# Kernel tuning notes

Hardware: AMD Instinct MI355X
Metric: run time of the kernel (lower is better)

## Reference

```python
import jax, jax.numpy as jnp
import numpy as np

# Irreps config: node = 64x0e + 32x1o, edge sh = 1x0e + 1x1o
N, E = 50000, 800000
MUL0, MUL1 = 64, 32
D_IN = MUL0 + 3 * MUL1          # 160
FC_H = 64
W_NUMEL = MUL0 + MUL0 + MUL1 + MUL1  # 192, per-instruction uvu weights
SQRT3 = 1.7320508075688772
ACT_C = 1.6791   # e3nn normalize2mom constant for silu


def setup_inputs() -> dict:
    key = jax.random.key(0)
    ks = jax.random.split(key, 11)
    return {
        "x": jax.random.normal(ks[0], (N, D_IN), jnp.float32),
        "edge_scalars": jax.random.uniform(ks[1], (E, FC_H), dtype=jnp.float32),
        "edge_attr_sh": jax.random.normal(ks[2], (E, 4), jnp.float32),
        "edge_index": jax.random.randint(ks[3], (2, E), 0, N),
        "w_fc1": jax.random.normal(ks[4], (FC_H, FC_H), jnp.float32),
        "w_fc2": jax.random.normal(ks[5], (FC_H, W_NUMEL), jnp.float32),
        "w_sc_s": jax.random.normal(ks[6], (MUL0, MUL0), jnp.float32),
        "w_sc_v": jax.random.normal(ks[7], (MUL1, MUL1), jnp.float32),
        "w_lin_s": jax.random.normal(ks[8], (96, MUL0), jnp.float32),
        "w_lin_v": jax.random.normal(ks[9], (96, MUL1), jnp.float32),
        "w_alpha": jax.random.normal(ks[10], (96, 1), jnp.float32) * 0.1,
    }


def reference(x, edge_scalars, edge_attr_sh, edge_index, w_fc1, w_fc2,
              w_sc_s, w_sc_v, w_lin_s, w_lin_v, w_alpha):
    src, dst = edge_index[0], edge_index[1]

    # --- fc: FullyConnectedNet([64, 64, 192], silu), e3nn fan-in norm ---
    h = jax.nn.silu(edge_scalars @ w_fc1 / np.sqrt(FC_H)) * ACT_C
    weight = h @ w_fc2 / np.sqrt(FC_H)                       # [E, 192]
    w0 = weight[:, :MUL0]                 # 0e x 0e -> 0e (mul 64)
    w1 = weight[:, MUL0:2 * MUL0]         # 0e x 1o -> 1o (mul 64)
    w2 = weight[:, 2 * MUL0:2 * MUL0 + MUL1]   # 1o x 0e -> 1o (mul 32)
    w3 = weight[:, 2 * MUL0 + MUL1:]           # 1o x 1o -> 0e (mul 32)

    # --- self connection: o3.Linear(in -> out), per-irrep mixing ---
    x_s = x[:, :MUL0]                                   # [N, 64]
    x_v = x[:, MUL0:].reshape(N, MUL1, 3)               # [N, 32, 3]
    sc_s = x_s @ w_sc_s / np.sqrt(MUL0)
    sc_v = jnp.einsum('nui,uw->nwi', x_v, w_sc_v) / np.sqrt(MUL1)
    sc_out = jnp.concatenate([sc_s, sc_v.reshape(N, 3 * MUL1)], axis=1)

    # --- gather + edge-weighted uvu tensor product ---
    gx_s = x_s[src]                                     # [E, 64]
    gx_v = x_v[src]                                     # [E, 32, 3]
    sh_s = edge_attr_sh[:, 0:1]                         # [E, 1]
    sh_v = edge_attr_sh[:, 1:4]                         # [E, 3]

    # path weights fold with w3j so factors cancel for 1o outputs
    mid_s0 = w0 * gx_s * sh_s                                        # [E,64] 0e
    mid_s1 = w3 * jnp.einsum('eui,ei->eu', gx_v, sh_v) / SQRT3       # [E,32] 0e
    mid_v0 = w1[:, :, None] * gx_s[:, :, None] * sh_v[:, None, :]    # [E,64,3] 1o
    mid_v1 = w2[:, :, None] * gx_v * sh_s[:, :, None]                # [E,32,3] 1o
    edge_feat = jnp.concatenate(
        [mid_s0, mid_s1, mid_v0.reshape(E, 3 * MUL0), mid_v1.reshape(E, 3 * MUL1)],
        axis=1)                                                      # [E, 384]

    # --- scatter-mean to destination nodes ---
    seg = jax.ops.segment_sum(edge_feat, dst, num_segments=N)
    cnt = jax.ops.segment_sum(jnp.ones((E,), edge_feat.dtype), dst, num_segments=N)
    mean = seg / jnp.maximum(cnt, 1.0)[:, None]                      # [N, 384]

    m_s = mean[:, :96]                                   # 96x0e
    m_v = mean[:, 96:].reshape(N, 96, 3)                 # 96x1o

    # --- alpha gate (o3.Linear mid -> 0e) and output linear ---
    alpha = m_s @ w_alpha / np.sqrt(96)                  # [N, 1]
    lin_s = m_s @ w_lin_s / np.sqrt(96)                  # [N, 64]
    lin_v = jnp.einsum('nui,uw->nwi', m_v, w_lin_v) / np.sqrt(96)
    lin_out = jnp.concatenate([lin_s, lin_v.reshape(N, 3 * MUL1)], axis=1)

    # sc.output_mask is all-ones here (every output irrep reachable)
    return sc_out + alpha * lin_out
```

## Files before the change

### kernel.cpp

```cpp
#include <hip/hip_runtime.h>
#include <hip/hip_bf16.h>

#define N_NODES 50000
#define N_EDGES 800000
#define MUL0 64
#define MUL1 32
#define D_IN 160
#define FC_H 64
#define W_NUMEL 192
#define FEAT 384
#define ACT_C 1.6791f
#define INV_SQRT3 0.57735026918962576f
#define RSQRT32 0.17677669529663687f
#define RSQRT96 0.10206207261596575f

#define TILE 32

typedef __attribute__((ext_vector_type(8))) short s16x8;
typedef __attribute__((ext_vector_type(4))) float f32x4;
typedef _Float16 h8 __attribute__((ext_vector_type(8)));
typedef __fp16 fp16x2 __attribute__((ext_vector_type(2)));

static __device__ __forceinline__ unsigned short f2bf(float f) {
    __hip_bfloat16 b = __float2bfloat16(f);
    return __builtin_bit_cast(unsigned short, b);
}

static __device__ __forceinline__ int swz(int row, int byte_in_row) {
    int unit = ((row & 1) << 2) | (byte_in_row >> 4);
    int su = unit ^ ((row >> 1) & 7);
    return (row >> 1) * 128 + su * 16 + (byte_in_row & 15);
}
static __device__ __forceinline__ h8 rdh8(const unsigned char* base, int row, int eb) {
    return *(const h8*)(base + swz(row, eb));
}


__global__ __launch_bounds__(256) void hist_kernel(const int* __restrict__ eidx,
                                                   int* __restrict__ cnt) {
    int e = blockIdx.x * 256 + threadIdx.x;
    if (e < N_EDGES) atomicAdd(&cnt[eidx[N_EDGES + e]], 1);
}

#define SCAN_NB 64
#define SCAN_CH ((N_NODES + SCAN_NB - 1) / SCAN_NB)

__global__ __launch_bounds__(256) void scanA_kernel(const int* __restrict__ cnt,
                                                    int* __restrict__ bsum) {
    __shared__ int sred[4];
    int b = blockIdx.x, t = threadIdx.x;
    int lim = min((b + 1) * SCAN_CH, N_NODES);
    int s = 0;
    for (int i = b * SCAN_CH + t; i < lim; i += 256) s += cnt[i];
    for (int d = 1; d < 64; d <<= 1) s += __shfl_xor(s, d);
    if ((t & 63) == 0) sred[t >> 6] = s;
    __syncthreads();
    if (t == 0) bsum[b] = sred[0] + sred[1] + sred[2] + sred[3];
}

__global__ __launch_bounds__(64) void scanB_kernel(const int* __restrict__ bsum,
                                                   int* __restrict__ boff) {
    int t = threadIdx.x;
    int v = bsum[t];
    int p = v;
    for (int d = 1; d < 64; d <<= 1) { int u = __shfl_up(p, d); if (t >= d) p += u; }
    boff[t] = p - v;
}

__global__ __launch_bounds__(256) void scanC_kernel(const int* __restrict__ cnt,
                                                    const int* __restrict__ boff,
                                                    int* __restrict__ fill) {
    __shared__ int s_w[4];
    int b = blockIdx.x, t = threadIdx.x;
    const int CH2 = (SCAN_CH + 255) / 256;
    int base = b * SCAN_CH + t * CH2;
    int lim = min((b + 1) * SCAN_CH, N_NODES);
    int s = 0;
#pragma unroll
    for (int k = 0; k < CH2; ++k) { int i = base + k; if (i < lim) s += cnt[i]; }
    int v = s;
    for (int d = 1; d < 64; d <<= 1) { int u = __shfl_up(v, d); if ((t & 63) >= d) v += u; }
    if ((t & 63) == 63) s_w[t >> 6] = v;
    __syncthreads();
    if (t == 0) { int run = 0; for (int w = 0; w < 4; ++w) { int tv = s_w[w]; s_w[w] = run; run += tv; } }
    __syncthreads();
    int run = boff[b] + s_w[t >> 6] + (v - s);
#pragma unroll
    for (int k = 0; k < CH2; ++k) {
        int i = base + k;
        if (i < lim) { fill[i] = run; run += cnt[i]; }
    }
}

__global__ __launch_bounds__(256) void scatter_ids_kernel(const int* __restrict__ eidx,
                                                          int* __restrict__ fill,
                                                          int* __restrict__ sorted_eid) {
    int e = blockIdx.x * 256 + threadIdx.x;
    if (e < N_EDGES) {
        int p = atomicAdd(&fill[eidx[N_EDGES + e]], 1);
        sorted_eid[p] = e;
    }
}

__global__ __launch_bounds__(256) void prep_w_kernel(
    const float* __restrict__ w_fc1,
    const float* __restrict__ w_fc2,
    const float* __restrict__ w_sc_s,
    const float* __restrict__ w_sc_v,
    const float* __restrict__ w_lin_s,
    const float* __restrict__ w_lin_v,
    unsigned short* __restrict__ w1t,
    unsigned short* __restrict__ w2t,
    unsigned short* __restrict__ wscs_t,
    unsigned short* __restrict__ wscv_t,
    unsigned short* __restrict__ wlins_t,
    unsigned short* __restrict__ wlinv_t)
{
    int i = blockIdx.x * 256 + threadIdx.x;
    if (i < 64 * 64)  w1t[i]    = f2bf(w_fc1[(i & 63) * FC_H + (i >> 6)]);
    if (i < 192 * 64) w2t[i]    = f2bf(w_fc2[(i & 63) * W_NUMEL + (i >> 6)]);
    if (i < 64 * 64)  wscs_t[i] = f2bf(w_sc_s[(i & 63) * 64 + (i >> 6)]);
    if (i < 32 * 32)  wscv_t[i] = f2bf(w_sc_v[(i & 31) * 32 + (i >> 5)]);
    if (i < 64 * 96)  wlins_t[i] = f2bf(w_lin_s[(i % 96) * 64 + (i / 96)]);
    if (i < 32 * 96)  wlinv_t[i] = f2bf(w_lin_v[(i % 96) * 32 + (i / 96)]);
}

#define X_OFF    0
#define W_OFF    10240
#define SH_OFF   22528
#define SID_OFF  22784
#define SEGN_OFF 22848
#define NSEG_OFF 22976
#define SMEM_SZ  22980

static __device__ __forceinline__ h8 seg_mask(const unsigned* vv, unsigned tgt) {
    h8 a;
#pragma unroll
    for (int w2 = 0; w2 < 4; ++w2) {
        a[w2 * 2]     = ((vv[w2] & 0xffffu) == tgt) ? (_Float16)1.f : (_Float16)0.f;
        a[w2 * 2 + 1] = ((vv[w2] >> 16)     == tgt) ? (_Float16)1.f : (_Float16)0.f;
    }
    return a;
}

__global__ __launch_bounds__(256) void edge_kernel(
    const float* __restrict__ x,
    const float* __restrict__ es,
    const float* __restrict__ sh,
    const int*   __restrict__ eidx,
    const int*   __restrict__ sorted_eid,
    const unsigned short* __restrict__ w1t,
    const unsigned short* __restrict__ w2t,
    float* __restrict__ accg)
{
    __shared__ __align__(16) unsigned char smem[SMEM_SZ];
    int* s_segnode = (int*)(smem + SEGN_OFF);
    unsigned short* s_sid = (unsigned short*)(smem + SID_OFF);

    const int t = threadIdx.x;
    const int l = t & 63;
    const int wv = t >> 6;
    const int lr = l & 15;
    const int lk = l >> 4;
    const int rg   = wv & 1;
    const int half = wv >> 1;
    const int tile0 = blockIdx.x * TILE;

    s16x8 w1b[2][2];
#pragma unroll
    for (int j = 0; j < 2; ++j)
#pragma unroll
        for (int kk = 0; kk < 2; ++kk)
            w1b[j][kk] = *(const s16x8*)(w1t + ((half * 2 + j) * 16 + lr) * 64 + kk * 32 + lk * 8);

    int eid_own = sorted_eid[tile0 + rg * 16 + lr];
    float4 esf[4];
    {
        const float4* ep = (const float4*)(es + (size_t)eid_own * FC_H);
        esf[0] = ep[lk * 2];     esf[1] = ep[lk * 2 + 1];
        esf[2] = ep[8 + lk * 2]; esf[3] = ep[8 + lk * 2 + 1];
    }
    const int xe = l & 31;
    const int xc0 = (wv * 2 + (l >> 5)) * 5;
    const int src_e = eidx[sorted_eid[tile0 + xe]];
    float4 xg[5];
    {
        const float4* xp = (const float4*)(x + (size_t)src_e * D_IN);
#pragma unroll
        for (int k = 0; k < 5; ++k) xg[k] = xp[xc0 + k];
    }
    float shv = 0.f;
    if (t < 128) shv = sh[(size_t)sorted_eid[tile0 + (t >> 2)] * 4 + (t & 3)];
    if (wv == 0) {
        int dl = (l < 32) ? eidx[N_EDGES + sorted_eid[tile0 + l]] : -1;
        int nd = __shfl_down(dl, 1);
        bool flag = (l == 31) || (l < 31 && dl != nd);
        unsigned long long m = __ballot(flag) & 0xffffffffull;
        int sid = __popcll(m & ((1ull << l) - 1ull));
        if (l < 32) {
            s_sid[l] = (unsigned short)sid;
            if (flag) s_segnode[sid] = dl;
            if (l == 31) *(int*)(smem + NSEG_OFF) = sid + 1;
        }
    }

    unsigned short* s_h = (unsigned short*)(smem + X_OFF);
    s16x8 afrag[2];
    {
        s16x8 a;
        a[0] = f2bf(esf[0].x); a[1] = f2bf(esf[0].y); a[2] = f2bf(esf[0].z); a[3] = f2bf(esf[0].w);
        a[4] = f2bf(esf[1].x); a[5] = f2bf(esf[1].y); a[6] = f2bf(esf[1].z); a[7] = f2bf(esf[1].w);
        afrag[0] = a;
        a[0] = f2bf(esf[2].x); a[1] = f2bf(esf[2].y); a[2] = f2bf(esf[2].z); a[3] = f2bf(esf[2].w);
        a[4] = f2bf(esf[3].x); a[5] = f2bf(esf[3].y); a[6] = f2bf(esf[3].z); a[7] = f2bf(esf[3].w);
        afrag[1] = a;
    }
#pragma unroll
    for (int j = 0; j < 2; ++j) {
        int nt = half * 2 + j;
        f32x4 hacc = {0.f, 0.f, 0.f, 0.f};
#pragma unroll
        for (int kk = 0; kk < 2; ++kk)
            hacc = __builtin_amdgcn_mfma_f32_16x16x32_bf16(afrag[kk], w1b[j][kk], hacc, 0, 0, 0);
#pragma unroll
        for (int q = 0; q < 4; ++q) {
            float aa = hacc[q] * 0.125f;
            float hv = aa * (1.f / (1.f + __expf(-aa))) * ACT_C;
            s_h[(rg * 16 + lk * 4 + q) * 72 + nt * 16 + lr] = f2bf(hv);
        }
    }
    __syncthreads();

    s16x8 hfrag[2];
#pragma unroll
    for (int kk = 0; kk < 2; ++kk)
        hfrag[kk] = *(const s16x8*)(s_h + (rg * 16 + lr) * 72 + kk * 32 + lk * 8);
    __syncthreads();

#pragma unroll
    for (int j = 0; j < 6; ++j) {
        int nt = half * 6 + j;
        f32x4 acc = {0.f, 0.f, 0.f, 0.f};
#pragma unroll
        for (int kk = 0; kk < 2; ++kk) {
            s16x8 b = *(const s16x8*)(w2t + (nt * 16 + lr) * 64 + kk * 32 + lk * 8);
            acc = __builtin_amdgcn_mfma_f32_16x16x32_bf16(hfrag[kk], b, acc, 0, 0, 0);
        }
        int f = nt * 16 + lr;
        fp16x2 p0 = __builtin_amdgcn_cvt_pkrtz(acc[0] * 0.125f, acc[1] * 0.125f);
        fp16x2 p1 = __builtin_amdgcn_cvt_pkrtz(acc[2] * 0.125f, acc[3] * 0.125f);
        uint2 wval = { __builtin_bit_cast(unsigned, p0), __builtin_bit_cast(unsigned, p1) };
        *(uint2*)(smem + W_OFF + swz(f, rg * 32 + lk * 8)) = wval;
    }
#pragma unroll
    for (int k = 0; k < 5; ++k) {
        float4 v = xg[k];
#pragma unroll
        for (int jj = 0; jj < 4; ++jj) {
            int r = (xc0 + k) * 4 + jj;
            float fv = (jj == 0) ? v.x : (jj == 1) ? v.y : (jj == 2) ? v.z : v.w;
            *(_Float16*)(smem + X_OFF + swz(r, xe * 2)) = (_Float16)fv;
        }
    }
    if (t < 128) {
        int e = t >> 2, c = t & 3;
        *(_Float16*)(smem + SH_OFF + swz(c, e * 2)) = (_Float16)shv;
    }
    __syncthreads();

    const int nseg = *(const int*)(smem + NSEG_OFF);
    const int eb = lk * 16;

    h8 shreg[4];
#pragma unroll
    for (int r = 0; r < 4; ++r) shreg[r] = rdh8(smem + SH_OFF, r, eb);
    uint4 sv = *(const uint4*)(smem + SID_OFF + eb);
    unsigned vv[4] = { sv.x, sv.y, sv.z, sv.w };

    h8 Bv[4];
    int fcol[4];
    bool cls3j[4] = {false, false, false, false};
    if (wv == 0) {
#pragma unroll
        for (int jj = 0; jj < 4; ++jj) {
            int col = jj * 16 + lr;
            Bv[jj] = rdh8(smem + W_OFF, col, eb) * rdh8(smem + X_OFF, col, eb);
            fcol[jj] = col;
        }
    } else if (wv == 1) {
#pragma unroll
        for (int jj = 0; jj < 4; ++jj) {
            int col = jj * 16 + lr;
            Bv[jj] = rdh8(smem + W_OFF, 128 + col / 3, eb) * rdh8(smem + X_OFF, 64 + col, eb);
            fcol[jj] = 288 + col;
        }
    } else if (wv == 2) {
#pragma unroll
        for (int jj = 0; jj < 2; ++jj) {
            int col = 64 + jj * 16 + lr;
            Bv[jj] = rdh8(smem + W_OFF, 128 + col / 3, eb) * rdh8(smem + X_OFF, 64 + col, eb);
            fcol[jj] = 288 + col;
        }
#pragma unroll
        for (int jj = 2; jj < 4; ++jj) {
            int col = (jj - 2) * 16 + lr;
            h8 d = rdh8(smem + X_OFF, 64 + 3 * col, eb)     * shreg[1]
                 + rdh8(smem + X_OFF, 64 + 3 * col + 1, eb) * shreg[2]
                 + rdh8(smem + X_OFF, 64 + 3 * col + 2, eb) * shreg[3];
            Bv[jj] = rdh8(smem + W_OFF, 160 + col, eb) * d;
            fcol[jj] = 64 + col;
            cls3j[jj] = true;
        }
    } else {
#pragma unroll
        for (int jj = 0; jj < 4; ++jj) {
            int col = jj * 16 + lr;
            Bv[jj] = rdh8(smem + W_OFF, 64 + col, eb) * rdh8(smem + X_OFF, col, eb);
            fcol[jj] = 96 + 3 * col;
        }
    }

    if (wv != 3) {
        const int npass = (nseg + 15) >> 4;
        for (int p = 0; p < npass; ++p) {
            h8 bm = seg_mask(vv, (unsigned)(p * 16 + lr));
            h8 Ash = bm * shreg[0];
            const int m0 = p * 16 + lk * 4;
            float* nptr[4]; bool valid[4], atq[4];
#pragma unroll
            for (int q = 0; q < 4; ++q) {
                int sg = m0 + q;
                valid[q] = sg < nseg;
                int node = valid[q] ? s_segnode[sg] : 0;
                nptr[q] = accg + (size_t)node * FEAT;
                atq[q] = (sg == 0) || (sg == nseg - 1);
            }
#pragma unroll
            for (int jj = 0; jj < 4; ++jj) {
                f32x4 acc = {0.f, 0.f, 0.f, 0.f};
                acc = __builtin_amdgcn_mfma_f32_16x16x32_f16(cls3j[jj] ? bm : Ash, Bv[jj], acc, 0, 0, 0);
                const float sc = cls3j[jj] ? INV_SQRT3 : 1.f;
#pragma unroll
                for (int q = 0; q < 4; ++q) {
                    if (valid[q]) {
                        float v = acc[q] * sc;
                        float* a = nptr[q] + fcol[jj];
                        if (atq[q]) atomicAdd(a, v); else *a = v;
                    }
                }
            }
        }
    } else {
        const int npass = (3 * nseg + 15) >> 4;
        for (int p = 0; p < npass; ++p) {
            int m = p * 16 + lr;
            int sgA = m / 3, i3A = m - 3 * sgA;
            h8 A = seg_mask(vv, (unsigned)sgA) *
                   ((i3A == 0) ? shreg[1] : (i3A == 1) ? shreg[2] : shreg[3]);
            int m0 = p * 16 + lk * 4;
            int sgq = m0 / 3, rq = m0 - 3 * sgq;
            float* nptr[4]; int i3q[4]; bool valid[4], atq[4];
#pragma unroll
            for (int q = 0; q < 4; ++q) {
                valid[q] = sgq < nseg;
                int node = valid[q] ? s_segnode[sgq] : 0;
                nptr[q] = accg + (size_t)node * FEAT;
                i3q[q] = rq;
                atq[q] = (sgq == 0) || (sgq == nseg - 1);
                if (++rq == 3) { rq = 0; ++sgq; }
            }
#pragma unroll
            for (int jj = 0; jj < 4; ++jj) {
                f32x4 acc = {0.f, 0.f, 0.f, 0.f};
                acc = __builtin_amdgcn_mfma_f32_16x16x32_f16(A, Bv[jj], acc, 0, 0, 0);
#pragma unroll
                for (int q = 0; q < 4; ++q) {
                    if (valid[q]) {
                        float* a = nptr[q] + fcol[jj] + i3q[q];
                        if (atq[q]) atomicAdd(a, acc[q]); else *a = acc[q];
                    }
                }
            }
        }
    }
}


static __device__ __forceinline__ s16x8 frag_c8(const float* p, float s) {
    float4 u = *(const float4*)p, v = *(const float4*)(p + 4);
    s16x8 a;
    a[0] = f2bf(u.x * s); a[1] = f2bf(u.y * s); a[2] = f2bf(u.z * s); a[3] = f2bf(u.w * s);
    a[4] = f2bf(v.x * s); a[5] = f2bf(v.y * s); a[6] = f2bf(v.z * s); a[7] = f2bf(v.w * s);
    return a;
}

__global__ __launch_bounds__(256) void node_kernel(
    const float* __restrict__ x,
    const float* __restrict__ accg,
    const int*   __restrict__ cnt,
    const unsigned short* __restrict__ wscs_t,
    const unsigned short* __restrict__ wscv_t,
    const unsigned short* __restrict__ wlins_t,
    const unsigned short* __restrict__ wlinv_t,
    const float* __restrict__ w_alpha,
    float* __restrict__ out)
{
    const int t = threadIdx.x;
    const int wv = t >> 6, l = t & 63;
    const int lr = l & 15, lk = l >> 4;
    const int n_base = blockIdx.x * 64 + wv * 16;
    const int nrow = n_base + lr;
    const int nclamp = min(nrow, N_NODES - 1);

    const float* mrow = accg + (size_t)nclamp * FEAT;
    const float* xrow = x + (size_t)nclamp * D_IN;
    const float rinv = 1.f / (float)max(cnt[nclamp], 1);

    s16x8 ax[2], ams[3], axv[3], amv[3][3];
#pragma unroll
    for (int kk = 0; kk < 2; ++kk) ax[kk] = frag_c8(xrow + kk * 32 + lk * 8, 1.f);
#pragma unroll
    for (int kk = 0; kk < 3; ++kk) ams[kk] = frag_c8(mrow + kk * 32 + lk * 8, rinv);
    {
        float xb[24];
        const float4* p = (const float4*)(xrow + 64 + 24 * lk);
#pragma unroll
        for (int q = 0; q < 6; ++q) ((float4*)xb)[q] = p[q];
#pragma unroll
        for (int i = 0; i < 3; ++i) {
            s16x8 a;
#pragma unroll
            for (int j = 0; j < 8; ++j) a[j] = f2bf(xb[3 * j + i]);
            axv[i] = a;
        }
    }
#pragma unroll
    for (int kk = 0; kk < 3; ++kk) {
        float mb[24];
        const float4* p = (const float4*)(mrow + 96 + 96 * kk + 24 * lk);
#pragma unroll
        for (int q = 0; q < 6; ++q) ((float4*)mb)[q] = p[q];
#pragma unroll
        for (int i = 0; i < 3; ++i) {
            s16x8 a;
#pragma unroll
            for (int j = 0; j < 8; ++j) a[j] = f2bf(mb[3 * j + i] * rinv);
            amv[i][kk] = a;
        }
    }

    float ap = 0.f;
    {
        float ab[24];
        const float4* p = (const float4*)(mrow + 24 * lk);
#pragma unroll
        for (int q = 0; q < 6; ++q) ((float4*)ab)[q] = p[q];
#pragma unroll
        for (int j = 0; j < 24; ++j) ap += ab[j] * rinv * w_alpha[lk * 24 + j];
    }
    ap += __shfl_xor(ap, 16);
    ap += __shfl_xor(ap, 32);
    const float alphav = ap * RSQRT96;

    f32x4 accA[4], accL[4];
#pragma unroll
    for (int nt = 0; nt < 4; ++nt) { accA[nt] = (f32x4){0,0,0,0}; accL[nt] = (f32x4){0,0,0,0}; }
#pragma unroll
    for (int nt = 0; nt < 4; ++nt) {
#pragma unroll
        for (int kk = 0; kk < 2; ++kk) {
            s16x8 b = *(const s16x8*)(wscs_t + (nt * 16 + lr) * 64 + kk * 32 + lk * 8);
            accA[nt] = __builtin_amdgcn_mfma_f32_16x16x32_bf16(ax[kk], b, accA[nt], 0, 0, 0);
        }
#pragma unroll
        for (int kk = 0; kk < 3; ++kk) {
            s16x8 b = *(const s16x8*)(wlins_t + (nt * 16 + lr) * 96 + kk * 32 + lk * 8);
            accL[nt] = __builtin_amdgcn_mfma_f32_16x16x32_bf16(ams[kk], b, accL[nt], 0, 0, 0);
        }
    }
    f32x4 accVs[3][2], accVl[3][2];
#pragma unroll
    for (int i = 0; i < 3; ++i)
#pragma unroll
        for (int nt = 0; nt < 2; ++nt) { accVs[i][nt] = (f32x4){0,0,0,0}; accVl[i][nt] = (f32x4){0,0,0,0}; }
#pragma unroll
    for (int i = 0; i < 3; ++i) {
#pragma unroll
        for (int nt = 0; nt < 2; ++nt) {
            s16x8 b = *(const s16x8*)(wscv_t + (nt * 16 + lr) * 32 + lk * 8);
            accVs[i][nt] = __builtin_amdgcn_mfma_f32_16x16x32_bf16(axv[i], b, accVs[i][nt], 0, 0, 0);
#pragma unroll
            for (int kk = 0; kk < 3; ++kk) {
                s16x8 b2 = *(const s16x8*)(wlinv_t + (nt * 16 + lr) * 96 + kk * 32 + lk * 8);
                accVl[i][nt] = __builtin_amdgcn_mfma_f32_16x16x32_bf16(amv[i][kk], b2, accVl[i][nt], 0, 0, 0);
            }
        }
    }

#pragma unroll
    for (int q = 0; q < 4; ++q) {
        int row = lk * 4 + q;
        float ar = __shfl(alphav, row);
        int n = n_base + row;
        bool ok = (n < N_NODES);
        float* orow = out + (size_t)n * 160;
#pragma unroll
        for (int nt = 0; nt < 4; ++nt) {
            float vout = accA[nt][q] * 0.125f + ar * accL[nt][q] * RSQRT96;
            if (ok) orow[nt * 16 + lr] = vout;
        }
#pragma unroll
        for (int i = 0; i < 3; ++i)
#pragma unroll
            for (int nt = 0; nt < 2; ++nt) {
                float vout = accVs[i][nt][q] * RSQRT32 + ar * accVl[i][nt][q] * RSQRT96;
                if (ok) orow[64 + 3 * (nt * 16 + lr) + i] = vout;
            }
    }
}


extern "C" void kernel_launch(void* const* d_in, const int* in_sizes, int n_in,
                              void* d_out, int out_size, void* d_ws, size_t ws_size,
                              hipStream_t stream) {
    const float* x        = (const float*)d_in[0];
    const float* es       = (const float*)d_in[1];
    const float* sh       = (const float*)d_in[2];
    const int*   eidx     = (const int*)d_in[3];
    const float* w_fc1    = (const float*)d_in[4];
    const float* w_fc2    = (const float*)d_in[5];
    const float* w_sc_s   = (const float*)d_in[6];
    const float* w_sc_v   = (const float*)d_in[7];
    const float* w_lin_s  = (const float*)d_in[8];
    const float* w_lin_v  = (const float*)d_in[9];
    const float* w_alpha  = (const float*)d_in[10];
    float* out = (float*)d_out;

    float* accg       = (float*)d_ws;
    int*   cnt        = (int*)(accg + (size_t)N_NODES * FEAT);
    int*   fill       = cnt + N_NODES;
    int*   sorted_eid = fill + N_NODES;
    unsigned short* w1t     = (unsigned short*)(sorted_eid + N_EDGES);
    unsigned short* w2t     = w1t + 64 * 64;
    unsigned short* wscs_t  = w2t + 192 * 64;
    unsigned short* wscv_t  = wscs_t + 64 * 64;
    unsigned short* wlins_t = wscv_t + 32 * 32;
    unsigned short* wlinv_t = wlins_t + 64 * 96;
    int* bsum = (int*)(wlinv_t + 32 * 96);
    int* boff = bsum + SCAN_NB;

    (void)hipMemsetAsync(d_ws, 0, ((size_t)N_NODES * FEAT + N_NODES) * 4, stream);
    hipLaunchKernelGGL(hist_kernel, dim3((N_EDGES + 255) / 256), dim3(256), 0, stream,
                       eidx, cnt);
    hipLaunchKernelGGL(scanA_kernel, dim3(SCAN_NB), dim3(256), 0, stream, cnt, bsum);
    hipLaunchKernelGGL(scanB_kernel, dim3(1), dim3(64), 0, stream, bsum, boff);
    hipLaunchKernelGGL(scanC_kernel, dim3(SCAN_NB), dim3(256), 0, stream, cnt, boff, fill);
    hipLaunchKernelGGL(scatter_ids_kernel, dim3((N_EDGES + 255) / 256), dim3(256), 0, stream,
                       eidx, fill, sorted_eid);
    hipLaunchKernelGGL(prep_w_kernel, dim3(48), dim3(256), 0, stream,
                       w_fc1, w_fc2, w_sc_s, w_sc_v, w_lin_s, w_lin_v,
                       w1t, w2t, wscs_t, wscv_t, wlins_t, wlinv_t);
    hipLaunchKernelGGL(edge_kernel, dim3(N_EDGES / TILE), dim3(256), 0, stream,
                       x, es, sh, eidx, sorted_eid, w1t, w2t, accg);
    hipLaunchKernelGGL(node_kernel, dim3((N_NODES + 63) / 64), dim3(256), 0, stream,
                       x, accg, cnt, wscs_t, wscv_t, wlins_t, wlinv_t, w_alpha, out);
}
```

Baseline: 475.1 us.

## Double edge tile to 64 edges per block with two-step K segment reduction

Raises the per-block edge tile from 32 to 64. Each wave now computes the fc MLP for its own 16-edge row group across all output columns, and the segment-reduction MFMA runs two K-steps over the 64 edges. The shared-memory swizzle and layout are reworked for 64-edge rows. The aim is fewer segments that straddle tile boundaries, so fewer atomics, and fewer blocks overall. In exchange the block roughly doubles its LDS footprint and register use, which may lower occupancy.

New measurement: 453.0 us. 1.05x faster.

```diff
diff --git a/kernel.cpp b/kernel.cpp
--- a/kernel.cpp
+++ b/kernel.cpp
@@ -14,7 +14,7 @@
 #define RSQRT32 0.17677669529663687f
 #define RSQRT96 0.10206207261596575f
 
-#define TILE 32
+#define TILE 64
 
 typedef __attribute__((ext_vector_type(8))) short s16x8;
 typedef __attribute__((ext_vector_type(4))) float f32x4;
@@ -27,9 +27,7 @@
 }
 
 static __device__ __forceinline__ int swz(int row, int byte_in_row) {
-    int unit = ((row & 1) << 2) | (byte_in_row >> 4);
-    int su = unit ^ ((row >> 1) & 7);
-    return (row >> 1) * 128 + su * 16 + (byte_in_row & 15);
+    return row * 128 + ((((byte_in_row >> 4) ^ (row & 7)) << 4) | (byte_in_row & 15));
 }
 static __device__ __forceinline__ h8 rdh8(const unsigned char* base, int row, int eb) {
     return *(const h8*)(base + swz(row, eb));
@@ -126,12 +124,12 @@
 }
 
 #define X_OFF    0
-#define W_OFF    10240
-#define SH_OFF   22528
-#define SID_OFF  22784
-#define SEGN_OFF 22848
-#define NSEG_OFF 22976
-#define SMEM_SZ  22980
+#define W_OFF    20480
+#define SH_OFF   45056
+#define SID_OFF  45568
+#define SEGN_OFF 45696
+#define NSEG_OFF 45952
+#define SMEM_SZ  45968
 
 static __device__ __forceinline__ h8 seg_mask(const unsigned* vv, unsigned tgt) {
     h8 a;
@@ -162,46 +160,35 @@
     const int wv = t >> 6;
     const int lr = l & 15;
     const int lk = l >> 4;
-    const int rg   = wv & 1;
-    const int half = wv >> 1;
     const int tile0 = blockIdx.x * TILE;
 
-    s16x8 w1b[2][2];
-#pragma unroll
-    for (int j = 0; j < 2; ++j)
-#pragma unroll
-        for (int kk = 0; kk < 2; ++kk)
-            w1b[j][kk] = *(const s16x8*)(w1t + ((half * 2 + j) * 16 + lr) * 64 + kk * 32 + lk * 8);
-
-    int eid_own = sorted_eid[tile0 + rg * 16 + lr];
+    int eid_own = sorted_eid[tile0 + wv * 16 + lr];
     float4 esf[4];
     {
         const float4* ep = (const float4*)(es + (size_t)eid_own * FC_H);
         esf[0] = ep[lk * 2];     esf[1] = ep[lk * 2 + 1];
         esf[2] = ep[8 + lk * 2]; esf[3] = ep[8 + lk * 2 + 1];
     }
-    const int xe = l & 31;
-    const int xc0 = (wv * 2 + (l >> 5)) * 5;
-    const int src_e = eidx[sorted_eid[tile0 + xe]];
-    float4 xg[5];
-    {
-        const float4* xp = (const float4*)(x + (size_t)src_e * D_IN);
-#pragma unroll
-        for (int k = 0; k < 5; ++k) xg[k] = xp[xc0 + k];
-    }
-    float shv = 0.f;
-    if (t < 128) shv = sh[(size_t)sorted_eid[tile0 + (t >> 2)] * 4 + (t & 3)];
+    float4 xg[10];
+    int xE[10], xC[10];
+#pragma unroll
+    for (int q = 0; q < 10; ++q) {
+        int i = q * 256 + t;
+        int e = i / 40, c4 = i - e * 40;
+        xE[q] = e; xC[q] = c4;
+        const float4* xp = (const float4*)(x + (size_t)eidx[sorted_eid[tile0 + e]] * D_IN);
+        xg[q] = xp[c4];
+    }
+    float shv = sh[(size_t)sorted_eid[tile0 + (t >> 2)] * 4 + (t & 3)];
     if (wv == 0) {
-        int dl = (l < 32) ? eidx[N_EDGES + sorted_eid[tile0 + l]] : -1;
+        int dl = eidx[N_EDGES + sorted_eid[tile0 + l]];
         int nd = __shfl_down(dl, 1);
-        bool flag = (l == 31) || (l < 31 && dl != nd);
-        unsigned long long m = __ballot(flag) & 0xffffffffull;
+        bool flag = (l == 63) || (dl != nd);
+        unsigned long long m = __ballot(flag);
         int sid = __popcll(m & ((1ull << l) - 1ull));
-        if (l < 32) {
-            s_sid[l] = (unsigned short)sid;
-            if (flag) s_segnode[sid] = dl;
-            if (l == 31) *(int*)(smem + NSEG_OFF) = sid + 1;
-        }
+        s_sid[l] = (unsigned short)sid;
+        if (flag) s_segnode[sid] = dl;
+        if (l == 63) *(int*)(smem + NSEG_OFF) = sid + 1;
     }
 
     unsigned short* s_h = (unsigned short*)(smem + X_OFF);
@@ -216,30 +203,28 @@
         afrag[1] = a;
     }
 #pragma unroll
-    for (int j = 0; j < 2; ++j) {
-        int nt = half * 2 + j;
+    for (int nt = 0; nt < 4; ++nt) {
         f32x4 hacc = {0.f, 0.f, 0.f, 0.f};
 #pragma unroll
-        for (int kk = 0; kk < 2; ++kk)
-            hacc = __builtin_amdgcn_mfma_f32_16x16x32_bf16(afrag[kk], w1b[j][kk], hacc, 0, 0, 0);
+        for (int kk = 0; kk < 2; ++kk) {
+            s16x8 b = *(const s16x8*)(w1t + (nt * 16 + lr) * 64 + kk * 32 + lk * 8);
+            hacc = __builtin_amdgcn_mfma_f32_16x16x32_bf16(afrag[kk], b, hacc, 0, 0, 0);
+        }
 #pragma unroll
         for (int q = 0; q < 4; ++q) {
             float aa = hacc[q] * 0.125f;
             float hv = aa * (1.f / (1.f + __expf(-aa))) * ACT_C;
-            s_h[(rg * 16 + lk * 4 + q) * 72 + nt * 16 + lr] = f2bf(hv);
-        }
-    }
+            s_h[(wv * 16 + lk * 4 + q) * 72 + nt * 16 + lr] = f2bf(hv);
+        }
+    }
+    s16x8 hfrag[2];
+#pragma unroll
+    for (int kk = 0; kk < 2; ++kk)
+        hfrag[kk] = *(const s16x8*)(s_h + (wv * 16 + lr) * 72 + kk * 32 + lk * 8);
     __syncthreads();
 
-    s16x8 hfrag[2];
-#pragma unroll
-    for (int kk = 0; kk < 2; ++kk)
-        hfrag[kk] = *(const s16x8*)(s_h + (rg * 16 + lr) * 72 + kk * 32 + lk * 8);
-    __syncthreads();
-
-#pragma unroll
-    for (int j = 0; j < 6; ++j) {
-        int nt = half * 6 + j;
+#pragma unroll
+    for (int nt = 0; nt < 12; ++nt) {
         f32x4 acc = {0.f, 0.f, 0.f, 0.f};
 #pragma unroll
         for (int kk = 0; kk < 2; ++kk) {
@@ -250,81 +235,93 @@
         fp16x2 p0 = __builtin_amdgcn_cvt_pkrtz(acc[0] * 0.125f, acc[1] * 0.125f);
         fp16x2 p1 = __builtin_amdgcn_cvt_pkrtz(acc[2] * 0.125f, acc[3] * 0.125f);
         uint2 wval = { __builtin_bit_cast(unsigned, p0), __builtin_bit_cast(unsigned, p1) };
-        *(uint2*)(smem + W_OFF + swz(f, rg * 32 + lk * 8)) = wval;
-    }
-#pragma unroll
-    for (int k = 0; k < 5; ++k) {
-        float4 v = xg[k];
+        *(uint2*)(smem + W_OFF + swz(f, wv * 32 + lk * 8)) = wval;
+    }
+#pragma unroll
+    for (int q = 0; q < 10; ++q) {
+        float4 v = xg[q];
 #pragma unroll
         for (int jj = 0; jj < 4; ++jj) {
-            int r = (xc0 + k) * 4 + jj;
+            int r = xC[q] * 4 + jj;
             float fv = (jj == 0) ? v.x : (jj == 1) ? v.y : (jj == 2) ? v.z : v.w;
-            *(_Float16*)(smem + X_OFF + swz(r, xe * 2)) = (_Float16)fv;
-        }
-    }
-    if (t < 128) {
+            *(_Float16*)(smem + X_OFF + swz(r, xE[q] * 2)) = (_Float16)fv;
+        }
+    }
+    {
         int e = t >> 2, c = t & 3;
         *(_Float16*)(smem + SH_OFF + swz(c, e * 2)) = (_Float16)shv;
     }
     __syncthreads();
 
     const int nseg = *(const int*)(smem + NSEG_OFF);
-    const int eb = lk * 16;
-
-    h8 shreg[4];
-#pragma unroll
-    for (int r = 0; r < 4; ++r) shreg[r] = rdh8(smem + SH_OFF, r, eb);
-    uint4 sv = *(const uint4*)(smem + SID_OFF + eb);
-    unsigned vv[4] = { sv.x, sv.y, sv.z, sv.w };
-
-    h8 Bv[4];
+
+    h8 shreg[4][2];
+#pragma unroll
+    for (int r = 0; r < 4; ++r)
+#pragma unroll
+        for (int ks = 0; ks < 2; ++ks)
+            shreg[r][ks] = rdh8(smem + SH_OFF, r, ks * 64 + lk * 16);
+    unsigned vv[2][4];
+#pragma unroll
+    for (int ks = 0; ks < 2; ++ks) {
+        uint4 sv = *(const uint4*)(smem + SID_OFF + ks * 64 + lk * 16);
+        vv[ks][0] = sv.x; vv[ks][1] = sv.y; vv[ks][2] = sv.z; vv[ks][3] = sv.w;
+    }
+
+    h8 Bv[4][2];
     int fcol[4];
     bool cls3j[4] = {false, false, false, false};
-    if (wv == 0) {
-#pragma unroll
-        for (int jj = 0; jj < 4; ++jj) {
-            int col = jj * 16 + lr;
-            Bv[jj] = rdh8(smem + W_OFF, col, eb) * rdh8(smem + X_OFF, col, eb);
-            fcol[jj] = col;
-        }
-    } else if (wv == 1) {
-#pragma unroll
-        for (int jj = 0; jj < 4; ++jj) {
-            int col = jj * 16 + lr;
-            Bv[jj] = rdh8(smem + W_OFF, 128 + col / 3, eb) * rdh8(smem + X_OFF, 64 + col, eb);
-            fcol[jj] = 288 + col;
-        }
-    } else if (wv == 2) {
-#pragma unroll
-        for (int jj = 0; jj < 2; ++jj) {
-            int col = 64 + jj * 16 + lr;
-            Bv[jj] = rdh8(smem + W_OFF, 128 + col / 3, eb) * rdh8(smem + X_OFF, 64 + col, eb);
-            fcol[jj] = 288 + col;
-        }
-#pragma unroll
-        for (int jj = 2; jj < 4; ++jj) {
-            int col = (jj - 2) * 16 + lr;
-            h8 d = rdh8(smem + X_OFF, 64 + 3 * col, eb)     * shreg[1]
-                 + rdh8(smem + X_OFF, 64 + 3 * col + 1, eb) * shreg[2]
-                 + rdh8(smem + X_OFF, 64 + 3 * col + 2, eb) * shreg[3];
-            Bv[jj] = rdh8(smem + W_OFF, 160 + col, eb) * d;
-            fcol[jj] = 64 + col;
-            cls3j[jj] = true;
-        }
-    } else {
-#pragma unroll
-        for (int jj = 0; jj < 4; ++jj) {
-            int col = jj * 16 + lr;
-            Bv[jj] = rdh8(smem + W_OFF, 64 + col, eb) * rdh8(smem + X_OFF, col, eb);
-            fcol[jj] = 96 + 3 * col;
+#pragma unroll
+    for (int ks = 0; ks < 2; ++ks) {
+        const int eb = ks * 64 + lk * 16;
+        if (wv == 0) {
+#pragma unroll
+            for (int jj = 0; jj < 4; ++jj) {
+                int col = jj * 16 + lr;
+                Bv[jj][ks] = rdh8(smem + W_OFF, col, eb) * rdh8(smem + X_OFF, col, eb);
+                fcol[jj] = col;
+            }
+        } else if (wv == 1) {
+#pragma unroll
+            for (int jj = 0; jj < 4; ++jj) {
+                int col = jj * 16 + lr;
+                Bv[jj][ks] = rdh8(smem + W_OFF, 128 + col / 3, eb) * rdh8(smem + X_OFF, 64 + col, eb);
+                fcol[jj] = 288 + col;
+            }
+        } else if (wv == 2) {
+#pragma unroll
+            for (int jj = 0; jj < 2; ++jj) {
+                int col = 64 + jj * 16 + lr;
+                Bv[jj][ks] = rdh8(smem + W_OFF, 128 + col / 3, eb) * rdh8(smem + X_OFF, 64 + col, eb);
+                fcol[jj] = 288 + col;
+            }
+#pragma unroll
+            for (int jj = 2; jj < 4; ++jj) {
+                int col = (jj - 2) * 16 + lr;
+                h8 d = rdh8(smem + X_OFF, 64 + 3 * col, eb)     * shreg[1][ks]
+                     + rdh8(smem + X_OFF, 64 + 3 * col + 1, eb) * shreg[2][ks]
+                     + rdh8(smem + X_OFF, 64 + 3 * col + 2, eb) * shreg[3][ks];
+                Bv[jj][ks] = rdh8(smem + W_OFF, 160 + col, eb) * d;
+                fcol[jj] = 64 + col;
+                cls3j[jj] = true;
+            }
+        } else {
+#pragma unroll
+            for (int jj = 0; jj < 4; ++jj) {
+                int col = jj * 16 + lr;
+                Bv[jj][ks] = rdh8(smem + W_OFF, 64 + col, eb) * rdh8(smem + X_OFF, col, eb);
+                fcol[jj] = 96 + 3 * col;
+            }
         }
     }
 
     if (wv != 3) {
         const int npass = (nseg + 15) >> 4;
         for (int p = 0; p < npass; ++p) {
-            h8 bm = seg_mask(vv, (unsigned)(p * 16 + lr));
-            h8 Ash = bm * shreg[0];
+            h8 bm0 = seg_mask(vv[0], (unsigned)(p * 16 + lr));
+            h8 bm1 = seg_mask(vv[1], (unsigned)(p * 16 + lr));
+            h8 As0 = bm0 * shreg[0][0];
+            h8 As1 = bm1 * shreg[0][1];
             const int m0 = p * 16 + lk * 4;
             float* nptr[4]; bool valid[4], atq[4];
 #pragma unroll
@@ -338,7 +335,8 @@
 #pragma unroll
             for (int jj = 0; jj < 4; ++jj) {
                 f32x4 acc = {0.f, 0.f, 0.f, 0.f};
-                acc = __builtin_amdgcn_mfma_f32_16x16x32_f16(cls3j[jj] ? bm : Ash, Bv[jj], acc, 0, 0, 0);
+                acc = __builtin_amdgcn_mfma_f32_16x16x32_f16(cls3j[jj] ? bm0 : As0, Bv[jj][0], acc, 0, 0, 0);
+                acc = __builtin_amdgcn_mfma_f32_16x16x32_f16(cls3j[jj] ? bm1 : As1, Bv[jj][1], acc, 0, 0, 0);
                 const float sc = cls3j[jj] ? INV_SQRT3 : 1.f;
 #pragma unroll
                 for (int q = 0; q < 4; ++q) {
@@ -355,8 +353,10 @@
         for (int p = 0; p < npass; ++p) {
             int m = p * 16 + lr;
             int sgA = m / 3, i3A = m - 3 * sgA;
-            h8 A = seg_mask(vv, (unsigned)sgA) *
-                   ((i3A == 0) ? shreg[1] : (i3A == 1) ? shreg[2] : shreg[3]);
+            h8 mk0 = seg_mask(vv[0], (unsigned)sgA);
+            h8 mk1 = seg_mask(vv[1], (unsigned)sgA);
+            h8 A0 = mk0 * ((i3A == 0) ? shreg[1][0] : (i3A == 1) ? shreg[2][0] : shreg[3][0]);
+            h8 A1 = mk1 * ((i3A == 0) ? shreg[1][1] : (i3A == 1) ? shreg[2][1] : shreg[3][1]);
             int m0 = p * 16 + lk * 4;
             int sgq = m0 / 3, rq = m0 - 3 * sgq;
             float* nptr[4]; int i3q[4]; bool valid[4], atq[4];
@@ -372,7 +372,8 @@
 #pragma unroll
             for (int jj = 0; jj < 4; ++jj) {
                 f32x4 acc = {0.f, 0.f, 0.f, 0.f};
-                acc = __builtin_amdgcn_mfma_f32_16x16x32_f16(A, Bv[jj], acc, 0, 0, 0);
+                acc = __builtin_amdgcn_mfma_f32_16x16x32_f16(A0, Bv[jj][0], acc, 0, 0, 0);
+                acc = __builtin_amdgcn_mfma_f32_16x16x32_f16(A1, Bv[jj][1], acc, 0, 0, 0);
 #pragma unroll
                 for (int q = 0; q < 4; ++q) {
                     if (valid[q]) {
```
